# Optimization experiments

Measured on AMD Instinct MI355X. Metric: run time of the kernel, lower is better.

The kernel has to match this reference:

```python
import jax, jax.numpy as jnp
import numpy as np
import math

B, T, V, D, K, H, CH, BN = 8, 1024, 256, 4096, 8192, 512, 8, 256

def setup_inputs() -> dict:
    key = jax.random.key(0)
    ks = jax.random.split(key, 20)
    def n(k, shape, s=0.02):
        return jax.random.normal(k, shape, dtype=jnp.float32) * s
    cb = jnp.where(jax.random.normal(ks[0], (V, D)) >= 0, 1.0, -1.0).astype(jnp.float32)
    return dict(
        idx=jax.random.randint(ks[1], (B, T), 0, V),
        char_codebook=cb,
        log_decay=jnp.full((D,), math.log(0.95 / 0.05), dtype=jnp.float32),
        gate_w=n(ks[2], (D, 1)), gate_b=jnp.zeros((1,), jnp.float32),
        q_w=n(ks[3], (D, BN)), q_b=jnp.zeros((BN,), jnp.float32),
        k_w=n(ks[4], (D, BN)), k_b=jnp.zeros((BN,), jnp.float32),
        phrase_w=n(ks[5], (D, D)), phrase_b=jnp.zeros((D,), jnp.float32),
        mem_keys=n(ks[6], (K, D)), mem_values=n(ks[7], (K, H)),
        log_beta=jnp.asarray(math.log(D ** 0.5), dtype=jnp.float32),
        proj1_w=n(ks[8], (D, H)), proj1_b=jnp.zeros((H,), jnp.float32),
        proj2_w=n(ks[9], (H, H)), proj2_b=jnp.zeros((H,), jnp.float32),
        phr_proj_w=n(ks[10], (D, H)), phr_proj_b=jnp.zeros((H,), jnp.float32),
        res_embed=n(ks[11], (V, H)), pos_embed=n(ks[12], (1024, H)),
        ln_g=jnp.ones((3 * H,), jnp.float32), ln_b=jnp.zeros((3 * H,), jnp.float32),
        nav_w0=n(ks[13], (3 * H, H)), nav_b0=jnp.zeros((H,), jnp.float32),
        nav_w1=n(ks[14], (H, H)), nav_b1=jnp.zeros((H,), jnp.float32),
        nav_w2=n(ks[15], (H, H)), nav_b2=jnp.zeros((H,), jnp.float32),
        head_w=n(ks[16], (H, V)), head_b=jnp.zeros((V,), jnp.float32),
    )

def reference(idx, char_codebook, log_decay, gate_w, gate_b, q_w, q_b, k_w, k_b,
              phrase_w, phrase_b, mem_keys, mem_values, log_beta,
              proj1_w, proj1_b, proj2_w, proj2_b, phr_proj_w, phr_proj_b,
              res_embed, pos_embed, ln_g, ln_b, nav_w0, nav_b0, nav_w1, nav_b1,
              nav_w2, nav_b2, head_w, head_b):
    gelu = lambda x: jax.nn.gelu(x, approximate=False)  # torch nn.GELU default (erf)
    # ---- trigram encoding: bind current char with rolled prev chars ----
    chars = char_codebook[idx]                                   # (B,T,D)
    c1 = jnp.roll(chars, 1, axis=1).at[:, 0, :].set(0.0)
    c2 = jnp.roll(chars, 2, axis=1).at[:, :2, :].set(0.0)
    tri = chars * jnp.roll(c1, 1, axis=-1) * jnp.roll(c2, 2, axis=-1)
    hdc = 0.7 * tri + 0.3 * chars
    # ---- build_context: gate + causal decay matrix + hetero resonance ----
    imp = jax.nn.sigmoid(hdc @ gate_w + gate_b)                  # (B,T,1)
    gated = hdc * imp
    ldr = jnp.mean(jax.nn.log_sigmoid(log_decay))
    i = jnp.arange(T)
    # faithful to source: diffs[t,s] = clamp(s - t, 0) -> tril of exp(ldr*0)=1
    diffs = jnp.clip(i[None, :] - i[:, None], 0, None).astype(jnp.float32)
    dm = jnp.tril(jnp.exp(ldr * diffs))
    dm = dm / (dm.sum(-1, keepdims=True) + 1e-8)                 # (T,T)
    local = jnp.einsum('ts,bsd->btd', dm, gated)
    q = gated @ q_w + q_b                                        # (B,T,BN)
    k = gated @ k_w + k_b
    scores = jnp.einsum('btc,bsc->bts', q, k) * (BN ** -0.5)
    res_mask = i[None, :] <= (i[:, None] - 4)                    # tril diagonal=-4
    scores = jnp.where(res_mask[None], scores, -65000.0)
    resonance = jax.nn.softmax(scores, axis=-1)
    combined = 0.7 * dm[None] + 0.3 * resonance
    hetero = jnp.einsum('bts,bsd->btd', combined, gated)
    contexts = 0.6 * local + 0.4 * hetero + hdc                  # (B,T,D)
    # ---- phrase level: chunk-8 pool, proj, causal decay over chunks ----
    nC = T // CH
    phrase = contexts.reshape(B, nC, CH, D).mean(2) @ phrase_w + phrase_b
    p = jnp.arange(nC)
    pdiff = jnp.clip(p[:, None] - p[None, :], 0, None).astype(jnp.float32)
    pm = jnp.tril(0.9 ** pdiff)
    pm = pm / pm.sum(-1, keepdims=True)
    phrase_ctx = jnp.einsum('ts,bsd->btd', pm, phrase)
    phrase_tok = jnp.repeat(phrase_ctx, CH, axis=1)              # (B,T,D)
    # ---- 3-step iterative Hopfield retrieval over codebook ----
    beta = jnp.exp(log_beta)
    qh = contexts
    for _ in range(3):
        attn = jax.nn.softmax(jnp.einsum('btd,kd->btk', qh, mem_keys) * beta, axis=-1)
        qh = jnp.einsum('btk,kd->btd', attn, mem_keys)
    retrieved = jnp.einsum('btk,kh->bth', attn, mem_values)      # (B,T,H)
    # ---- features + navigator (eval: dropout identity, n_thoughts=1) ----
    f_char = gelu(contexts @ proj1_w + proj1_b) @ proj2_w + proj2_b + retrieved
    f_phr = phrase_tok @ phr_proj_w + phr_proj_b
    f_res = res_embed[idx] + pos_embed[:T][None]
    x = jnp.concatenate([f_char, f_phr, f_res], axis=-1)         # (B,T,3H)
    mu = x.mean(-1, keepdims=True)
    var = ((x - mu) ** 2).mean(-1, keepdims=True)
    xh = (x - mu) / jnp.sqrt(var + 1e-5) * ln_g + ln_b
    h = gelu(xh @ nav_w0 + nav_b0)
    h = gelu(h @ nav_w1 + nav_b1)
    h = gelu(h @ nav_w2 + nav_b2)
    return h @ head_w + head_b                                   # (B,T,V)
```

## Files before the change

kernel.cpp:

```cpp
#include <hip/hip_runtime.h>
#include <cstdint>
#include <cstddef>


using u16 = unsigned short;
typedef __bf16 bf16x8 __attribute__((ext_vector_type(8)));
typedef float  f32x4  __attribute__((ext_vector_type(4)));

#define DEV __device__ __forceinline__

DEV float u2f(u16 u) { return __uint_as_float(((unsigned)u) << 16); }
DEV u16   f2u(float f) {
    unsigned x = __float_as_uint(f);
    return (u16)((x + 0x7fffu + ((x >> 16) & 1u)) >> 16);
}
DEV float gelu_f(float v) { return 0.5f * v * (1.0f + erff(v * 0.70710678118654752440f)); }

enum : int { Tt_ = 1024, Dd_ = 4096, Kk_ = 8192, Hh_ = 512, NC_ = 128, H3_ = 1536 };

template<int OUTK, int BIAS, int GELU, int ADD, int AS, int BS, int BTR>
__global__ __launch_bounds__(256) void gemm_u(
    const void* __restrict__ Av, const void* __restrict__ Av2, long sA, int ldA,
    const void* __restrict__ Bv, const void* __restrict__ Bv2, long sB, int ldB,
    void* __restrict__ Cv, void* __restrict__ Cv2, long sC, int ldC,
// ... 135 lines not shown
        #pragma unroll
        for (int n = 0; n < 4; ++n)
            bh[n] = *(const bf16x8*)&Bs_hi[(wc * 64 + n * 16 + fr) * 32 + fq * 8];
        if constexpr (AS >= 2) {
            #pragma unroll
            for (int m = 0; m < 4; ++m)
                al[m] = *(const bf16x8*)&As_lo[(wr * 64 + m * 16 + fr) * 32 + fq * 8];
        }
        if constexpr (BS >= 2) {
            #pragma unroll
            for (int n = 0; n < 4; ++n)
                bl[n] = *(const bf16x8*)&Bs_lo[(wc * 64 + n * 16 + fr) * 32 + fq * 8];
        }
        #pragma unroll
        for (int m = 0; m < 4; ++m)
            #pragma unroll
            for (int n = 0; n < 4; ++n)
                acc[m][n] = __builtin_amdgcn_mfma_f32_16x16x32_bf16(ah[m], bh[n], acc[m][n], 0, 0, 0);
        if constexpr (AS >= 2) {
            #pragma unroll
            for (int m = 0; m < 4; ++m)
                #pragma unroll
                for (int n = 0; n < 4; ++n)
                    acc[m][n] = __builtin_amdgcn_mfma_f32_16x16x32_bf16(al[m], bh[n], acc[m][n], 0, 0, 0);
        }
        if constexpr (BS >= 2) {
            #pragma unroll
            for (int m = 0; m < 4; ++m)
                #pragma unroll
                for (int n = 0; n < 4; ++n)
                    acc[m][n] = __builtin_amdgcn_mfma_f32_16x16x32_bf16(ah[m], bl[n], acc[m][n], 0, 0, 0);
        }
        __syncthreads();
    }

    float alf = alpha;
    if (alpha_exp) alf *= expf(*alpha_exp);
    const long r0 = arow0 + wr * 64;
    const int  c0 = (int)brow0 + wc * 64;
    const long cbase = (long)blockIdx.z * sC;
    const long dbase = (long)blockIdx.z * sAdd;
    float* Cf = (float*)Cv;
    u16*   Ch = (u16*)Cv;
    u16*   Cl = (u16*)Cv2;
    #pragma unroll
    for (int m = 0; m < 4; ++m) {
        #pragma unroll
        for (int n = 0; n < 4; ++n) {
            const int c = c0 + n * 16 + fr;
            #pragma unroll
            for (int i = 0; i < 4; ++i) {
                const long r = r0 + m * 16 + fq * 4 + i;
                float v = acc[m][n][i] * alf;
                if (BIAS == 1) v += bias[c];
                if (BIAS == 2) v += bias[r];
                if (ADD)  v += addsrc[dbase + r * (long)ldC + c];
                if (GELU) v = gelu_f(v);
                const long o = cbase + r * (long)ldC + c;
                if (OUTK == 0) Cf[o] = v;
                else if (OUTK == 1) Ch[o] = f2u(v);
                else { const u16 h = f2u(v); Ch[o] = h; Cl[o] = f2u(v - u2f(h)); }
            }
        }
    }
}

__global__ __launch_bounds__(256) void gemm_sym(
    const u16* __restrict__ A, u16* __restrict__ G, int N, int Kc)
{
    __shared__ u16 As[128 * 32];
    __shared__ u16 Bs[128 * 32];
    __shared__ u16 tile[128][129];

    int f = blockIdx.x;
    {
        const int nwg = gridDim.x;
        if (nwg >= 16) {
            const int q = nwg >> 3, r = nwg & 7;
            const int xcd = f & 7, pos = f >> 3;
            f = (xcd < r) ? (xcd * (q + 1) + pos)
                          : (r * (q + 1) + (xcd - r) * q + pos);
        }
    }
    int bx = (int)((sqrtf(8.f * (float)f + 1.f) - 1.f) * 0.5f);
    while ((bx + 1) * (bx + 2) / 2 <= f) ++bx;
    while (bx * (bx + 1) / 2 > f) --bx;
    const int by = f - bx * (bx + 1) / 2;

    const int tid = threadIdx.x, lane = tid & 63, wave = tid >> 6;
    const int wr = wave >> 1, wc = wave & 1;
    const int fr = lane & 15, fq = lane >> 4;
    const int srow = tid >> 2, scol = (tid & 3) << 3;
    const u16* Ab = A + ((long)bx * 128 + srow) * Kc + scol;
    const u16* Bg = A + ((long)by * 128 + srow) * Kc + scol;
    u16* asd = &As[srow * 32 + scol];
    u16* bsd = &Bs[srow * 32 + scol];

    f32x4 acc[4][4] = {};
    for (int k0 = 0; k0 < Kc; k0 += 32) {
        __builtin_amdgcn_global_load_lds((const __attribute__((address_space(1))) void*)(Ab + k0),
                                         (__attribute__((address_space(3))) void*)asd, 16, 0, 0);
        __builtin_amdgcn_global_load_lds((const __attribute__((address_space(1))) void*)(Ab + k0 + (long)64 * Kc),
                                         (__attribute__((address_space(3))) void*)(asd + 64 * 32), 16, 0, 0);
        __builtin_amdgcn_global_load_lds((const __attribute__((address_space(1))) void*)(Bg + k0),
                                         (__attribute__((address_space(3))) void*)bsd, 16, 0, 0);
        __builtin_amdgcn_global_load_lds((const __attribute__((address_space(1))) void*)(Bg + k0 + (long)64 * Kc),
                                         (__attribute__((address_space(3))) void*)(bsd + 64 * 32), 16, 0, 0);
        __syncthreads();
        bf16x8 af[4], bv[4];
        #pragma unroll
        for (int m = 0; m < 4; ++m)
            af[m] = *(const bf16x8*)&As[(wr * 64 + m * 16 + fr) * 32 + fq * 8];
        #pragma unroll
        for (int n = 0; n < 4; ++n)
            bv[n] = *(const bf16x8*)&Bs[(wc * 64 + n * 16 + fr) * 32 + fq * 8];
        #pragma unroll
        for (int m = 0; m < 4; ++m)
            #pragma unroll
            for (int n = 0; n < 4; ++n)
                acc[m][n] = __builtin_amdgcn_mfma_f32_16x16x32_bf16(af[m], bv[n], acc[m][n], 0, 0, 0);
        __syncthreads();
    }

    const long rB = (long)bx * 128, cB = (long)by * 128;
    #pragma unroll
    for (int m = 0; m < 4; ++m) {
        #pragma unroll
        for (int n = 0; n < 4; ++n) {
            const int cl = wc * 64 + n * 16 + fr;
            #pragma unroll
            for (int i = 0; i < 4; ++i) {
                const int rl = wr * 64 + m * 16 + fq * 4 + i;
                const u16 h = f2u(acc[m][n][i]);
                G[(rB + rl) * (long)N + cB + cl] = h;
                tile[rl][cl] = h;
            }
        }
    }
    if (bx != by) {
        __syncthreads();
        const int rl2 = (tid & 63) * 2;
        #pragma unroll
        for (int j = 0; j < 32; ++j) {
            const int cl2 = (tid >> 6) + j * 4;
            const unsigned v = (unsigned)tile[rl2][cl2] | ((unsigned)tile[rl2 + 1][cl2] << 16);
            *(unsigned*)&G[(cB + cl2) * (long)N + rB + rl2] = v;
        }
    }
}

__global__ __launch_bounds__(256) void transpose_cast(
    const float* __restrict__ src, u16* __restrict__ dst, int R, int C)
{
    __shared__ float tile[32][33];
    const int c0 = blockIdx.x * 32, r0 = blockIdx.y * 32;
    const int tx = threadIdx.x & 31, ty = threadIdx.x >> 5;
    #pragma unroll
    for (int i = ty; i < 32; i += 8)
        tile[i][tx] = src[(long)(r0 + i) * C + c0 + tx];
    __syncthreads();
    #pragma unroll
    for (int i = ty; i < 32; i += 8)
        dst[(long)(c0 + i) * R + r0 + tx] = f2u(tile[tx][i]);
}

__global__ __launch_bounds__(256) void transpose_split(
    const float* __restrict__ src, u16* __restrict__ dhi, u16* __restrict__ dlo,
    int R, int C)
{
    __shared__ float tile[32][33];
// ... 59 lines not shown
        const float s0 = c0[d];
        float tri = 0.f;
        if (i2 >= 0) {
            const float s1 = c1[(d + Dd_ - 1) & (Dd_ - 1)];
            const float s2 = c2[(d + Dd_ - 2) & (Dd_ - 1)];
            tri = s0 * s1 * s2;
        }
        const float h = 0.7f * tri + 0.3f * s0;
        hv[j] = h;
        part += h * gate_w[d];
    }
    red[threadIdx.x] = part; __syncthreads();
    for (int q = 128; q > 0; q >>= 1) { if (threadIdx.x < q) red[threadIdx.x] += red[threadIdx.x + q]; __syncthreads(); }
    const float imp = 1.f / (1.f + expf(-(red[0] + gate_b[0])));
    if (threadIdx.x == 0) impOut[n] = imp;
    #pragma unroll
    for (int j = 0; j < 16; ++j) {
        const int d = threadIdx.x + j * 256;
        const float v = hv[j] * imp;
        const u16 h = f2u(v);
        gh[(long)n * Dd_ + d] = h;
        gl[(long)n * Dd_ + d] = f2u(v - u2f(h));
    }
}

__global__ __launch_bounds__(256) void seg_sum_pair(
    const u16* __restrict__ gh, const u16* __restrict__ gl, float* __restrict__ segsum)
{
    const int d = blockIdx.x * 256 + threadIdx.x;
    const int seg = blockIdx.y;
    const int b = blockIdx.z;
    const long base = ((long)b * Tt_ + seg * 64) * Dd_ + d;
    float s = 0.f;
    #pragma unroll 8
    for (int r = 0; r < 64; ++r) s += u2f(gh[base + (long)r * Dd_]) + u2f(gl[base + (long)r * Dd_]);
    segsum[((long)b * 16 + seg) * Dd_ + d] = s;
}

__global__ __launch_bounds__(256) void cum_base(
    const u16* __restrict__ gh, const u16* __restrict__ gl,
    const float* __restrict__ segsum, const float* __restrict__ imp,
    float* __restrict__ base, int b0)
{
    const int d = blockIdx.x * 256 + threadIdx.x;
    const int seg = blockIdx.y;
    const int b = b0 + blockIdx.z;
    float acc = 0.f;
    for (int s = 0; s < seg; ++s) acc += segsum[((long)b * 16 + s) * Dd_ + d];
    const long gbase = ((long)b * Tt_ + seg * 64) * Dd_ + d;
    const float* impb = imp + b * Tt_ + seg * 64;
    float* o = base + ((long)blockIdx.z * Tt_ + seg * 64) * Dd_ + d;
    for (int r = 0; r < 64; ++r) {
        const float g = u2f(gh[gbase + (long)r * Dd_]) + u2f(gl[gbase + (long)r * Dd_]);
        acc += g;
        const int t = seg * 64 + r;
        const float local = acc / (float)(t + 1);
        o[(long)r * Dd_] = g / impb[r] + 0.88f * local;
    }
}

__global__ __launch_bounds__(256) void softmax_res_pair(
    const float* __restrict__ scores, u16* __restrict__ rh, u16* __restrict__ rl)
{
    __shared__ float ex[Tt_];
    __shared__ float red[256];
    const int row = blockIdx.x;
    const int t = row & (Tt_ - 1);
    const int tid = threadIdx.x;
    const float* s = scores + (long)row * Tt_;
    u16* oh = rh + (long)row * Tt_;
    u16* ol = rl + (long)row * Tt_;
    if (t < 4) {
        const u16 u = f2u(1.f / 1024.f);
        for (int j = tid; j < Tt_; j += 256) { oh[j] = u; ol[j] = 0; }
        return;
    }
    const int nv = t - 3;
    float mx = -3.0e38f;
    for (int j = tid; j < nv; j += 256) { float v = s[j]; ex[j] = v; mx = fmaxf(mx, v); }
    red[tid] = mx; __syncthreads();
    for (int q = 128; q > 0; q >>= 1) { if (tid < q) red[tid] = fmaxf(red[tid], red[tid + q]); __syncthreads(); }
    const float MX = red[0]; __syncthreads();
    float sum = 0.f;
    for (int j = tid; j < nv; j += 256) { float e = expf(ex[j] - MX); ex[j] = e; sum += e; }
    red[tid] = sum; __syncthreads();
    for (int q = 128; q > 0; q >>= 1) { if (tid < q) red[tid] += red[tid + q]; __syncthreads(); }
    const float inv = 1.f / red[0];
    for (int j = tid; j < nv; j += 256) {
        const float p = ex[j] * inv;
        const u16 h = f2u(p);
        oh[j] = h; ol[j] = f2u(p - u2f(h));
    }
    for (int j = nv + tid; j < Tt_; j += 256) { oh[j] = 0; ol[j] = 0; }
}

__global__ __launch_bounds__(256) void diag_k(
    const float* __restrict__ mk, float* __restrict__ dex)
{
    __shared__ float red[256];
    const int row = blockIdx.x;
    const float* src = mk + (long)row * Dd_;
    float s = 0.f;
    #pragma unroll
    for (int j = 0; j < 16; ++j) { const float x = src[threadIdx.x + j * 256]; s += x * x; }
    red[threadIdx.x] = s; __syncthreads();
    for (int q = 128; q > 0; q >>= 1) { if (threadIdx.x < q) red[threadIdx.x] += red[threadIdx.x + q]; __syncthreads(); }
    if (threadIdx.x == 0) dex[row] = red[0];
}

__global__ __launch_bounds__(256) void select_refine(
    const float* __restrict__ S, const u16* __restrict__ chi,
    const u16* __restrict__ clo, const float* __restrict__ mk,
    const float* __restrict__ log_beta,
    int* __restrict__ cnt, int* __restrict__ idxb, float* __restrict__ wb)
{
    __shared__ float ex[Kk_];
    __shared__ float red[256];
    __shared__ int   ridx[256];
    __shared__ int   cidx[128];
    __shared__ float ce[128];
    __shared__ int   ccnt_s;
    const int tid = threadIdx.x;
    const int row = blockIdx.x;
    const float* s = S + (long)row * Kk_;
    float mx = -3.0e38f; int mi = 0;
    for (int j = tid; j < Kk_; j += 256) {
        const float v = s[j]; ex[j] = v;
        if (v > mx) { mx = v; mi = j; }
    }
    red[tid] = mx; ridx[tid] = mi; __syncthreads();
    for (int q = 128; q > 0; q >>= 1) {
        if (tid < q) {
            if (red[tid + q] > red[tid] ||
                (red[tid + q] == red[tid] && ridx[tid + q] < ridx[tid])) {
                red[tid] = red[tid + q]; ridx[tid] = ridx[tid + q];
            }
        }
        __syncthreads();
    }
    const float MXH = red[0];
    const int   AMX = ridx[0];
    __syncthreads();
    if (tid == 0) cidx[0] = AMX;
    if (tid < 64) {
        int c = 1;
        for (int base = 0; base < Kk_; base += 64) {
            const int col = base + tid;
            const bool keep = (ex[col] >= MXH - 16.0f) && (col != AMX);
            const unsigned long long m = __ballot(keep);
            if (keep) {
                const int pos = c + (int)__popcll(m & ((1ull << tid) - 1ull));
                if (pos < 128) cidx[pos] = col;
            }
            c += (int)__popcll(m);
        }
        if (tid == 0) ccnt_s = (c < 128) ? c : 128;
    }
    __syncthreads();
    const int kc = ccnt_s;
    const long cb = (long)row * Dd_;
    float av[16];
    #pragma unroll
    for (int j = 0; j < 16; ++j) {
        const int d = tid + j * 256;
        av[j] = u2f(chi[cb + d]) + u2f(clo[cb + d]);
    }
    const float beta = expf(*log_beta);
    for (int i = 0; i < kc; ++i) {
        const float* kr = mk + (long)cidx[i] * Dd_;
        float p = 0.f;
        #pragma unroll
        for (int j = 0; j < 16; ++j) p += av[j] * kr[tid + j * 256];
        red[tid] = p; __syncthreads();
        for (int q = 128; q > 0; q >>= 1) { if (tid < q) red[tid] += red[tid + q]; __syncthreads(); }
        if (tid == 0) ce[i] = beta * red[0];
        __syncthreads();
    }
    red[tid] = (tid < kc) ? ce[tid] : -3.0e38f;
    __syncthreads();
    for (int q = 128; q > 0; q >>= 1) { if (tid < q) red[tid] = fmaxf(red[tid], red[tid + q]); __syncthreads(); }
    const float M = red[0]; __syncthreads();
    float sum = 0.f;
    for (int j = tid; j < Kk_; j += 256) sum += expf(ex[j] - M);
    red[tid] = sum; __syncthreads();
    for (int q = 128; q > 0; q >>= 1) { if (tid < q) red[tid] += red[tid + q]; __syncthreads(); }
    float D = red[0]; __syncthreads();
    red[tid] = (tid < kc) ? (expf(ce[tid] - M) - expf(ex[cidx[tid]] - M)) : 0.f;
    __syncthreads();
    for (int q = 128; q > 0; q >>= 1) { if (tid < q) red[tid] += red[tid + q]; __syncthreads(); }
    D += red[0];
    const float invD = 1.f / D;
    if (tid < 64) {
        int c = 0;
        int*   oi = idxb + (long)row * 64;
        float* ow = wb   + (long)row * 64;
        for (int base = 0; base < 128; base += 64) {
            const int i = base + tid;
            const float w = (i < kc) ? expf(ce[i] - M) * invD : 0.f;
            const bool keep = (w > 1e-4f);
            const unsigned long long m = __ballot(keep);
            if (keep) {
                const int pos = c + (int)__popcll(m & ((1ull << tid) - 1ull));
                if (pos < 64) { oi[pos] = cidx[i]; ow[pos] = w; }
            }
            c += (int)__popcll(m);
        }
        if (tid == 0) cnt[row] = (c < 64) ? c : 64;
    }
}

__global__ __launch_bounds__(256) void gram_iter(
    const int* __restrict__ cntI, const int* __restrict__ idxI,
    const float* __restrict__ wI, const u16* __restrict__ G,
    const float* __restrict__ dex, const float* __restrict__ log_beta,
    int* __restrict__ cntO, int* __restrict__ idxO, float* __restrict__ wO)
{
    __shared__ float ex[Kk_];
    __shared__ float red[256];
    const int row = blockIdx.x;
    const int tid = threadIdx.x;
    const float beta = expf(*log_beta);
    const int k = cntI[row];
    float v[32];
    #pragma unroll
    for (int j = 0; j < 32; ++j) v[j] = 0.f;
    for (int i = 0; i < k; ++i) {
        const int   id = idxI[row * 64 + i];
        const float w  = wI[row * 64 + i];
        const u16* g = G + (long)id * Kk_;
        #pragma unroll
        for (int j = 0; j < 32; ++j)
            v[j] += w * u2f(g[tid + j * 256]);
    }
    #pragma unroll
    for (int j = 0; j < 32; ++j) ex[tid + j * 256] = beta * v[j];
    __syncthreads();
    if (tid < k) {
        const int   id = idxI[row * 64 + tid];
        const float w  = wI[row * 64 + tid];
        ex[id] += beta * w * (dex[id] - u2f(G[(long)id * Kk_ + id]));
    }
    __syncthreads();
    float mx = -3.0e38f;
    #pragma unroll
    for (int j = 0; j < 32; ++j) mx = fmaxf(mx, ex[tid + j * 256]);
    red[tid] = mx; __syncthreads();
    for (int q = 128; q > 0; q >>= 1) { if (tid < q) red[tid] = fmaxf(red[tid], red[tid + q]); __syncthreads(); }
    const float MX = red[0]; __syncthreads();
    float sum = 0.f;
    #pragma unroll
    for (int j = 0; j < 32; ++j) {
        const float e = expf(ex[tid + j * 256] - MX);
        ex[tid + j * 256] = e;
        sum += e;
    }
    red[tid] = sum; __syncthreads();
    for (int q = 128; q > 0; q >>= 1) { if (tid < q) red[tid] += red[tid + q]; __syncthreads(); }
    const float inv = 1.f / red[0];
    if (tid < 64) {
        int c = 0;
        int*   oi = idxO + row * 64;
        float* ow = wO   + row * 64;
        for (int base = 0; base < Kk_; base += 64) {
            const float w = ex[base + tid] * inv;
            const bool  keep = (w > 1e-4f);
            const unsigned long long m = __ballot(keep);
            if (keep) {
                const int pos = c + (int)__popcll(m & ((1ull << tid) - 1ull));
                if (pos < 64) { oi[pos] = base + tid; ow[pos] = w; }
            }
            c += (int)__popcll(m);
        }
        if (tid == 0) cntO[row] = (c < 64) ? c : 64;
    }
}

__global__ __launch_bounds__(256) void gather_value(
    const int* __restrict__ cnt, const int* __restrict__ idxb,
    const float* __restrict__ wb, const float* __restrict__ mv,
    float* __restrict__ fchar)
{
    const int row = blockIdx.x;
    const int k = cnt[row];
    float a0 = 0.f, a1 = 0.f;
    for (int i = 0; i < k; ++i) {
        const int   id = idxb[row * 64 + i];
        const float w  = wb[row * 64 + i];
        const float* src = mv + (long)id * Hh_;
        a0 += w * src[threadIdx.x];
        a1 += w * src[threadIdx.x + 256];
    }
    float* o = fchar + (long)row * Hh_;
    o[threadIdx.x]       += a0;
    o[threadIdx.x + 256] += a1;
}

__global__ __launch_bounds__(256) void hdc_gate(
    const int* __restrict__ idx, const float* __restrict__ cb,
    const float* __restrict__ gate_w, const float* __restrict__ gate_b,
    float* __restrict__ gated, int b)
{
    __shared__ float red[256];
    const int t = blockIdx.x;
    const int n = b * Tt_ + t;
    const int i0 = idx[n];
    const int i2 = (t >= 2) ? idx[n - 2] : -1;
    const int i1 = (t >= 1) ? idx[n - 1] : 0;
    const float* c0 = cb + (long)i0 * Dd_;
    const float* c1 = cb + (long)i1 * Dd_;
    const float* c2 = (i2 >= 0) ? cb + (long)i2 * Dd_ : cb;
    float hv[16];
    float part = 0.f;
    #pragma unroll
    for (int j = 0; j < 16; ++j) {
        const int d = threadIdx.x + j * 256;
        const float s0 = c0[d];
        float tri = 0.f;
        if (i2 >= 0) {
            const float s1 = c1[(d + Dd_ - 1) & (Dd_ - 1)];
            const float s2 = c2[(d + Dd_ - 2) & (Dd_ - 1)];
            tri = s0 * s1 * s2;
        }
        const float h = 0.7f * tri + 0.3f * s0;
        hv[j] = h;
        part += h * gate_w[d];
    }
    red[threadIdx.x] = part; __syncthreads();
    for (int q = 128; q > 0; q >>= 1) { if (threadIdx.x < q) red[threadIdx.x] += red[threadIdx.x + q]; __syncthreads(); }
    const float imp = 1.f / (1.f + expf(-(red[0] + gate_b[0])));
    #pragma unroll
    for (int j = 0; j < 16; ++j) {
        const int d = threadIdx.x + j * 256;
        gated[(long)t * Dd_ + d] = hv[j] * imp;
    }
}
// ... 175 lines not shown
    for (int j = tid; j < H3_; j += 256) { float d0 = xs[j] - mu; v += d0 * d0; }
    red[tid] = v; __syncthreads();
    for (int q = 128; q > 0; q >>= 1) { if (tid < q) red[tid] += red[tid + q]; __syncthreads(); }
    const float rstd = rsqrtf(red[0] * (1.f / (float)H3_) + 1e-5f);
    u16* xo = x + (long)n * H3_;
    for (int j = tid; j < H3_; j += 256)
        xo[j] = f2u((xs[j] - mu) * rstd * ln_g[j] + ln_b[j]);
}

__global__ void fill_sentinel(float* o, long n, float val) {
    long i = (long)blockIdx.x * 256 + threadIdx.x;
    if (i < n) o[i] = val;
}

template<int OUTK, int BIAS, int GELU, int ADD, int AS, int BS, int BTR>
static void gemm(hipStream_t st,
                 const void* A, const void* A2, long sA, int ldA,
                 const void* B, const void* B2, long sB, int ldB,
                 void* C, void* C2, long sC, int ldC,
                 const float* bias, const float* add, long sAdd,
                 int M, int Ncols, int Kc, int batch, float alpha, const float* aexp)
{
    dim3 g(M / 128, Ncols / 128, batch), blk(256, 1, 1);
    gemm_u<OUTK, BIAS, GELU, ADD, AS, BS, BTR><<<g, blk, 0, st>>>(
        A, A2, sA, ldA, B, B2, sB, ldB, C, C2, sC, ldC, bias, add, sAdd, Kc, alpha, aexp);
}

struct Args {
    const int* idx; const float* cb;
    const float* gate_w; const float* gate_b;
    const float* q_w; const float* q_b; const float* k_w; const float* k_b;
    const float* phrase_w; const float* phrase_b;
    const float* mem_keys; const float* mem_values; const float* log_beta;
    const float* proj1_w; const float* proj1_b;
    const float* proj2_w; const float* proj2_b;
    const float* phr_proj_w; const float* phr_proj_b;
    const float* res_embed; const float* pos_embed;
    const float* ln_g; const float* ln_b;
    const float* nav_w0; const float* nav_b0;
    const float* nav_w1; const float* nav_b1;
    const float* nav_w2; const float* nav_b2;
    const float* head_w; const float* head_b;
};

static void run_fast(const Args& a, void* d_out, char* ws, hipStream_t stream)
{
    const size_t MB = 1048576;
    u16* p1T    = (u16*)(ws + 0 * MB);
    u16* ppT    = (u16*)(ws + 4 * MB);
    u16* p2T    = (u16*)(ws + 8 * MB);
    u16* n0T    = (u16*)(ws + 8 * MB + 524288);
    u16* n1T    = (u16*)(ws + 10 * MB);
    u16* n2T    = (u16*)(ws + 10 * MB + 524288);
    u16* hT     = (u16*)(ws + 11 * MB);
    float* qkb  = (float*)(ws + 11 * MB + 524288);
    u16* qkwTh  = (u16*)(ws + 12 * MB);
    u16* qkwTl  = (u16*)(ws + 16 * MB);
    float* fphr  = (float*)(ws + 20 * MB);
    float* fchar = (float*)(ws + 22 * MB);
    u16* gb_hi  = (u16*)(ws + 38 * MB);
    u16* gb_lo  = (u16*)(ws + 102 * MB);
    u16* ctx_hi = gb_hi;
    u16* ctx_lo = gb_lo;
    u16* gbT_hi = (u16*)(ws + 166 * MB);
    u16* gbT_lo = (u16*)(ws + 230 * MB);
    u16* phwT   = (u16*)(ws + 166 * MB);
    u16* mk_hi  = (u16*)(ws + 166 * MB);
    u16* x      = (u16*)(ws + 166 * MB);
    u16* h1     = (u16*)(ws + 190 * MB);
    u16* h2     = (u16*)(ws + 198 * MB);
    u16* h3     = (u16*)(ws + 206 * MB);
    float* qkT   = (float*)(ws + 294 * MB);
    u16*   qk_hi = (u16*)(ws + 310 * MB);
    u16*   qk_lo = (u16*)(ws + 318 * MB);
    float* scores= (float*)(ws + 326 * MB);
    float* segs  = (float*)(ws + 358 * MB);
    u16*   rs_hi = (u16*)(ws + 360 * MB);
    u16*   rs_lo = (u16*)(ws + 376 * MB);
    float* base  = (float*)(ws + 294 * MB);
    u16* pool    = (u16*)(ws + 392 * MB);
    u16* phrase  = (u16*)(ws + 400 * MB);
    u16* pctx    = (u16*)(ws + 408 * MB);
    u16* t1      = (u16*)(ws + 416 * MB);
    float* S     = (float*)(ws + 358 * MB);
    u16*   G     = (u16*)(ws + 294 * MB);
    int*   selcA = (int*)(ws + 424 * MB);
    int*   selcB = (int*)(ws + 424 * MB + 262144);
    int*   seliA = (int*)(ws + 425 * MB);
    float* selwA = (float*)(ws + 427 * MB);
    int*   seliB = (int*)(ws + 429 * MB);
    float* selwB = (float*)(ws + 431 * MB);
    float* dexact= (float*)(ws + 433 * MB);
    float* impA  = (float*)(ws + 433 * MB + 32768);

    transpose_cast<<<dim3(16, 128), 256, 0, stream>>>(a.proj1_w, p1T, 4096, 512);
    transpose_cast<<<dim3(16, 16), 256, 0, stream>>>(a.proj2_w, p2T, 512, 512);
    transpose_cast<<<dim3(16, 128), 256, 0, stream>>>(a.phr_proj_w, ppT, 4096, 512);
    transpose_cast<<<dim3(16, 48), 256, 0, stream>>>(a.nav_w0, n0T, 1536, 512);
    transpose_cast<<<dim3(16, 16), 256, 0, stream>>>(a.nav_w1, n1T, 512, 512);
    transpose_cast<<<dim3(16, 16), 256, 0, stream>>>(a.nav_w2, n2T, 512, 512);
    transpose_cast<<<dim3(8, 16), 256, 0, stream>>>(a.head_w, hT, 512, 256);
    transpose_split<<<dim3(8, 128), 256, 0, stream>>>(a.q_w, qkwTh, qkwTl, 4096, 256);
    transpose_split<<<dim3(8, 128), 256, 0, stream>>>(a.k_w, qkwTh + (size_t)256 * 4096,
                                                      qkwTl + (size_t)256 * 4096, 4096, 256);
    hipMemcpyAsync(qkb, a.q_b, 256 * sizeof(float), hipMemcpyDeviceToDevice, stream);
    hipMemcpyAsync(qkb + 256, a.k_b, 256 * sizeof(float), hipMemcpyDeviceToDevice, stream);

    hdc_gate_pair<<<8192, 256, 0, stream>>>(a.idx, a.cb, a.gate_w, a.gate_b,
                                            gb_hi, gb_lo, impA);
    transpose_b2b<<<dim3(128, 32, 8), 256, 0, stream>>>(gb_hi, gbT_hi, 1024, 4096,
                                                        (long)1024 * 4096, (long)4096 * 1024);
    transpose_b2b<<<dim3(128, 32, 8), 256, 0, stream>>>(gb_lo, gbT_lo, 1024, 4096,
                                                        (long)1024 * 4096, (long)4096 * 1024);
    gemm<0, 2, 0, 0, 3, 3, 0>(stream, qkwTh, qkwTl, 0, 4096, gb_hi, gb_lo, 0, 4096,
                              qkT, nullptr, 0, 8192, qkb, nullptr, 0,
                              512, 8192, 4096, 1, 1.0f, nullptr);
    transpose_split<<<dim3(256, 16), 256, 0, stream>>>(qkT, qk_hi, qk_lo, 512, 8192);
    gemm<0, 0, 0, 0, 3, 3, 0>(stream, qk_hi, qk_lo, (long)1024 * 512, 512,
                              qk_hi + 256, qk_lo + 256, (long)1024 * 512, 512,
                              scores, nullptr, (long)1024 * 1024, 1024, nullptr, nullptr, 0,
                              1024, 1024, 256, 8, 0.0625f, nullptr);
    softmax_res_pair<<<8192, 256, 0, stream>>>(scores, rs_hi, rs_lo);
    seg_sum_pair<<<dim3(16, 16, 8), 256, 0, stream>>>(gb_hi, gb_lo, segs);
    for (int h = 0; h < 2; ++h) {
        cum_base<<<dim3(16, 16, 4), 256, 0, stream>>>(gb_hi, gb_lo, segs, impA,
                                                      base, h * 4);
        const long co = (long)h * 4 * 1024 * 4096;
        gemm<2, 0, 0, 1, 3, 3, 0>(stream,
                                  rs_hi + (long)h * 4 * 1024 * 1024,
                                  rs_lo + (long)h * 4 * 1024 * 1024, (long)1024 * 1024, 1024,
                                  gbT_hi + (long)h * 4 * 4096 * 1024,
                                  gbT_lo + (long)h * 4 * 4096 * 1024, (long)4096 * 1024, 1024,
                                  ctx_hi + co, ctx_lo + co, (long)1024 * 4096, 4096,
                                  nullptr, base, (long)1024 * 4096,
                                  1024, 4096, 1024, 4, 0.12f, nullptr);
    }

    pool_b<<<16384, 256, 0, stream>>>(ctx_hi, pool);
    transpose_cast<<<dim3(128, 128), 256, 0, stream>>>(a.phrase_w, phwT, 4096, 4096);
    gemm<1, 1, 0, 0, 0, 0, 0>(stream, pool, nullptr, 0, 4096, phwT, nullptr, 0, 4096,
                              phrase, nullptr, 0, 4096, a.phrase_b, nullptr, 0,
                              1024, 4096, 4096, 1, 1.0f, nullptr);
    phrase_decay<<<128, 256, 0, stream>>>(phrase, pctx);
    gemm<0, 1, 0, 0, 0, 0, 0>(stream, pctx, nullptr, 0, 4096, ppT, nullptr, 0, 4096,
                              fphr, nullptr, 0, 512, a.phr_proj_b, nullptr, 0,
                              1024, 512, 4096, 1, 1.0f, nullptr);

    gemm<1, 1, 1, 0, 0, 0, 0>(stream, ctx_hi, nullptr, 0, 4096, p1T, nullptr, 0, 4096,
                              t1, nullptr, 0, 512, a.proj1_b, nullptr, 0,
                              8192, 512, 4096, 1, 1.0f, nullptr);
    gemm<0, 1, 0, 0, 0, 0, 0>(stream, t1, nullptr, 0, 512, p2T, nullptr, 0, 512,
                              fchar, nullptr, 0, 512, a.proj2_b, nullptr, 0,
                              8192, 512, 512, 1, 1.0f, nullptr);

    cast_hi<<<32768, 256, 0, stream>>>(a.mem_keys, mk_hi, (long)8192 * 4096);
    diag_k<<<8192, 256, 0, stream>>>(a.mem_keys, dexact);

    for (int c = 0; c < 4; ++c) {
        u16* chi = ctx_hi + (long)c * 2048 * 4096;
        u16* clo = ctx_lo + (long)c * 2048 * 4096;
        gemm<0, 0, 0, 0, 0, 0, 0>(stream, chi, nullptr, 0, 4096, mk_hi, nullptr, 0, 4096,
                                  S, nullptr, 0, 8192, nullptr, nullptr, 0,
                                  2048, 8192, 4096, 1, 1.0f, a.log_beta);
        select_refine<<<2048, 256, 0, stream>>>(S, chi, clo, a.mem_keys, a.log_beta,
                                                selcA + c * 2048,
                                                seliA + (long)c * 2048 * 64,
                                                selwA + (long)c * 2048 * 64);
    }

    gemm_sym<<<2080, 256, 0, stream>>>(mk_hi, G, 8192, 4096);
    gram_iter<<<8192, 256, 0, stream>>>(selcA, seliA, selwA, G, dexact, a.log_beta,
                                        selcB, seliB, selwB);
    gram_iter<<<8192, 256, 0, stream>>>(selcB, seliB, selwB, G, dexact, a.log_beta,
                                        selcA, seliA, selwA);
    gather_value<<<8192, 256, 0, stream>>>(selcA, seliA, selwA, a.mem_values, fchar);

    concat_ln<<<8192, 256, 0, stream>>>(fchar, fphr, a.idx, a.res_embed, a.pos_embed,
                                        a.ln_g, a.ln_b, x);
    gemm<1, 1, 1, 0, 0, 0, 0>(stream, x, nullptr, 0, 1536, n0T, nullptr, 0, 1536,
                              h1, nullptr, 0, 512, a.nav_b0, nullptr, 0,
                              8192, 512, 1536, 1, 1.0f, nullptr);
    gemm<1, 1, 1, 0, 0, 0, 0>(stream, h1, nullptr, 0, 512, n1T, nullptr, 0, 512,
                              h2, nullptr, 0, 512, a.nav_b1, nullptr, 0,
                              8192, 512, 512, 1, 1.0f, nullptr);
    gemm<1, 1, 1, 0, 0, 0, 0>(stream, h2, nullptr, 0, 512, n2T, nullptr, 0, 512,
                              h3, nullptr, 0, 512, a.nav_b2, nullptr, 0,
                              8192, 512, 512, 1, 1.0f, nullptr);
    gemm<0, 1, 0, 0, 0, 0, 0>(stream, h3, nullptr, 0, 512, hT, nullptr, 0, 512,
                              d_out, nullptr, 0, 256, a.head_b, nullptr, 0,
                              8192, 256, 512, 1, 1.0f, nullptr);
}

static void run_fallback(const Args& a, void* d_out, char* ws, hipStream_t stream)
{
    const size_t o_p1T   = 0;
    const size_t o_ppT   = 4194304;
    const size_t o_p2T   = 8388608;
    const size_t o_n0T   = 8912896;
    const size_t o_n1T   = 10485760;
    const size_t o_n2T   = 11010048;
    const size_t o_hT    = 11534336;
    const size_t o_fphr  = 11796480;
    const size_t o_fchar = 13893632;
    const size_t o_ctx   = 30670848;
    const size_t o_AR    = 164888576;

    float* ctxf  = (float*)(ws + o_ctx);
    float* fchar = (float*)(ws + o_fchar);
    float* fphr  = (float*)(ws + o_fphr);
    float* gatedb = (float*)(ws + o_AR);
    float* localb = (float*)(ws + o_AR + 16777216);
    float* Rb     = (float*)(ws + o_AR + 33554432);
    float* qf     = (float*)(ws + o_AR + 50331648);
    float* kf     = (float*)(ws + o_AR + 51380224);
    float* segs   = (float*)(ws + o_AR + 52428800);
    float* scores = (float*)(ws + o_AR + 53477376);
    float* reso   = (float*)(ws + o_AR + 57671680);
    u16* pool   = (u16*)(ws + o_AR);
    u16* phrase = (u16*)(ws + o_AR + 8388608);
    u16* pctx   = (u16*)(ws + o_AR + 16777216);
    u16*   t1   = (u16*)(ws + o_AR);
    float* S    = (float*)(ws + o_AR);
    u16*   attn = (u16*)(ws + o_AR + 33554432);
    u16*   x    = (u16*)(ws + o_AR);
    u16*   h1   = (u16*)(ws + o_AR + 25165824);
    u16*   h2   = (u16*)(ws + o_AR + 33554432);
    u16*   h3   = (u16*)(ws + o_AR + 41943040);

    transpose_cast<<<dim3(16, 128), 256, 0, stream>>>(a.proj1_w, (u16*)(ws + o_p1T), 4096, 512);
    transpose_cast<<<dim3(16, 16), 256, 0, stream>>>(a.proj2_w, (u16*)(ws + o_p2T), 512, 512);
    transpose_cast<<<dim3(16, 128), 256, 0, stream>>>(a.phr_proj_w, (u16*)(ws + o_ppT), 4096, 512);
    transpose_cast<<<dim3(16, 48), 256, 0, stream>>>(a.nav_w0, (u16*)(ws + o_n0T), 1536, 512);
    transpose_cast<<<dim3(16, 16), 256, 0, stream>>>(a.nav_w1, (u16*)(ws + o_n1T), 512, 512);
    transpose_cast<<<dim3(16, 16), 256, 0, stream>>>(a.nav_w2, (u16*)(ws + o_n2T), 512, 512);
    transpose_cast<<<dim3(8, 16), 256, 0, stream>>>(a.head_w, (u16*)(ws + o_hT), 512, 256);

    for (int b = 0; b < 8; ++b) {
        hdc_gate<<<1024, 256, 0, stream>>>(a.idx, a.cb, a.gate_w, a.gate_b, gatedb, b);
        gemm<0, 1, 0, 0, 2, 2, 1>(stream, gatedb, nullptr, 0, 4096, a.q_w, nullptr, 0, 256,
                                  qf, nullptr, 0, 256, a.q_b, nullptr, 0,
                                  1024, 256, 4096, 1, 1.0f, nullptr);
        gemm<0, 1, 0, 0, 2, 2, 1>(stream, gatedb, nullptr, 0, 4096, a.k_w, nullptr, 0, 256,
                                  kf, nullptr, 0, 256, a.k_b, nullptr, 0,
                                  1024, 256, 4096, 1, 1.0f, nullptr);
        gemm<0, 0, 0, 0, 2, 2, 0>(stream, qf, nullptr, 0, 256, kf, nullptr, 0, 256,
                                  scores, nullptr, 0, 1024, nullptr, nullptr, 0,
                                  1024, 1024, 256, 1, 0.0625f, nullptr);
        softmax_res<<<1024, 256, 0, stream>>>(scores, reso);
        gemm<0, 0, 0, 0, 2, 2, 1>(stream, reso, nullptr, 0, 1024, gatedb, nullptr, 0, 4096,
                                  Rb, nullptr, 0, 4096, nullptr, nullptr, 0,
                                  1024, 4096, 1024, 1, 1.0f, nullptr);
// ... 116 lines not shown
```

Baseline: 3.164 ms.

## Store Hopfield scores in bf16, merge chunked score GEMM, retile symmetric Gram blocks

The score matrix between contexts and memory keys is now written as bf16 instead of fp32. That halves its size, so the four chunked GEMM plus select_refine passes become one full-batch GEMM and one select_refine launch, with the buffer reusing the Gram region. The symmetric Gram kernel maps block indices through 8x8 super-tiles for better L2 locality, and the softmax paths switch expf to __expf. Because bf16 scores are less precise, the candidate window is widened from 16 to 18 to keep the refinement correct, at some accuracy risk.

```diff
diff --git a/kernel.cpp b/kernel.cpp
--- a/kernel.cpp
+++ b/kernel.cpp
@@ -241,10 +241,27 @@
                           : (r * (q + 1) + (xcd - r) * q + pos);
         }
     }
-    int bx = (int)((sqrtf(8.f * (float)f + 1.f) - 1.f) * 0.5f);
-    while ((bx + 1) * (bx + 2) / 2 <= f) ++bx;
-    while (bx * (bx + 1) / 2 > f) --bx;
-    const int by = f - bx * (bx + 1) / 2;
+    int I = 0, J = 0, local = f;
+    {
+        bool done = false;
+        for (int i = 0; i < 8 && !done; ++i) {
+            for (int j = 0; j <= i; ++j) {
+                const int sz = (i == j) ? 36 : 64;
+                if (local < sz) { I = i; J = j; done = true; break; }
+                local -= sz;
+            }
+        }
+    }
+    int bx, by;
+    if (I == J) {
+        int r = 0;
+        while ((r + 1) * (r + 2) / 2 <= local) ++r;
+        bx = I * 8 + r;
+        by = J * 8 + (local - r * (r + 1) / 2);
+    } else {
+        bx = I * 8 + (local >> 3);
+        by = J * 8 + (local & 7);
+    }
 
     const int tid = threadIdx.x, lane = tid & 63, wave = tid >> 6;
     const int wr = wave >> 1, wc = wave & 1;
@@ -470,7 +487,7 @@
     for (int q = 128; q > 0; q >>= 1) { if (tid < q) red[tid] = fmaxf(red[tid], red[tid + q]); __syncthreads(); }
     const float MX = red[0]; __syncthreads();
     float sum = 0.f;
-    for (int j = tid; j < nv; j += 256) { float e = expf(ex[j] - MX); ex[j] = e; sum += e; }
+    for (int j = tid; j < nv; j += 256) { float e = __expf(ex[j] - MX); ex[j] = e; sum += e; }
     red[tid] = sum; __syncthreads();
     for (int q = 128; q > 0; q >>= 1) { if (tid < q) red[tid] += red[tid + q]; __syncthreads(); }
     const float inv = 1.f / red[0];
@@ -497,7 +514,7 @@
 }
 
 __global__ __launch_bounds__(256) void select_refine(
-    const float* __restrict__ S, const u16* __restrict__ chi,
+    const u16* __restrict__ S, const u16* __restrict__ chi,
     const u16* __restrict__ clo, const float* __restrict__ mk,
     const float* __restrict__ log_beta,
     int* __restrict__ cnt, int* __restrict__ idxb, float* __restrict__ wb)
@@ -510,10 +527,10 @@
     __shared__ int   ccnt_s;
     const int tid = threadIdx.x;
     const int row = blockIdx.x;
-    const float* s = S + (long)row * Kk_;
+    const u16* s = S + (long)row * Kk_;
     float mx = -3.0e38f; int mi = 0;
     for (int j = tid; j < Kk_; j += 256) {
-        const float v = s[j]; ex[j] = v;
+        const float v = u2f(s[j]); ex[j] = v;
         if (v > mx) { mx = v; mi = j; }
     }
     red[tid] = mx; ridx[tid] = mi; __syncthreads();
@@ -534,7 +551,7 @@
         int c = 1;
         for (int base = 0; base < Kk_; base += 64) {
             const int col = base + tid;
-            const bool keep = (ex[col] >= MXH - 16.0f) && (col != AMX);
+            const bool keep = (ex[col] >= MXH - 18.0f) && (col != AMX);
             const unsigned long long m = __ballot(keep);
             if (keep) {
                 const int pos = c + (int)__popcll(m & ((1ull << tid) - 1ull));
@@ -569,11 +586,11 @@
     for (int q = 128; q > 0; q >>= 1) { if (tid < q) red[tid] = fmaxf(red[tid], red[tid + q]); __syncthreads(); }
     const float M = red[0]; __syncthreads();
     float sum = 0.f;
-    for (int j = tid; j < Kk_; j += 256) sum += expf(ex[j] - M);
+    for (int j = tid; j < Kk_; j += 256) sum += __expf(ex[j] - M);
     red[tid] = sum; __syncthreads();
     for (int q = 128; q > 0; q >>= 1) { if (tid < q) red[tid] += red[tid + q]; __syncthreads(); }
     float D = red[0]; __syncthreads();
-    red[tid] = (tid < kc) ? (expf(ce[tid] - M) - expf(ex[cidx[tid]] - M)) : 0.f;
+    red[tid] = (tid < kc) ? (__expf(ce[tid] - M) - __expf(ex[cidx[tid]] - M)) : 0.f;
     __syncthreads();
     for (int q = 128; q > 0; q >>= 1) { if (tid < q) red[tid] += red[tid + q]; __syncthreads(); }
     D += red[0];
@@ -584,7 +601,7 @@
         float* ow = wb   + (long)row * 64;
         for (int base = 0; base < 128; base += 64) {
             const int i = base + tid;
-            const float w = (i < kc) ? expf(ce[i] - M) * invD : 0.f;
+            const float w = (i < kc) ? __expf(ce[i] - M) * invD : 0.f;
             const bool keep = (w > 1e-4f);
             const unsigned long long m = __ballot(keep);
             if (keep) {
@@ -638,7 +655,7 @@
     float sum = 0.f;
     #pragma unroll
     for (int j = 0; j < 32; ++j) {
-        const float e = expf(ex[tid + j * 256] - MX);
+        const float e = __expf(ex[tid + j * 256] - MX);
         ex[tid + j * 256] = e;
         sum += e;
     }
@@ -980,7 +997,7 @@
     u16* phrase  = (u16*)(ws + 400 * MB);
     u16* pctx    = (u16*)(ws + 408 * MB);
     u16* t1      = (u16*)(ws + 416 * MB);
-    float* S     = (float*)(ws + 358 * MB);
+    u16*   S16   = (u16*)(ws + 294 * MB);
     u16*   G     = (u16*)(ws + 294 * MB);
     int*   selcA = (int*)(ws + 424 * MB);
     int*   selcB = (int*)(ws + 424 * MB + 262144);
@@ -1054,17 +1071,11 @@
     cast_hi<<<32768, 256, 0, stream>>>(a.mem_keys, mk_hi, (long)8192 * 4096);
     diag_k<<<8192, 256, 0, stream>>>(a.mem_keys, dexact);
 
-    for (int c = 0; c < 4; ++c) {
-        u16* chi = ctx_hi + (long)c * 2048 * 4096;
-        u16* clo = ctx_lo + (long)c * 2048 * 4096;
-        gemm<0, 0, 0, 0, 0, 0, 0>(stream, chi, nullptr, 0, 4096, mk_hi, nullptr, 0, 4096,
-                                  S, nullptr, 0, 8192, nullptr, nullptr, 0,
-                                  2048, 8192, 4096, 1, 1.0f, a.log_beta);
-        select_refine<<<2048, 256, 0, stream>>>(S, chi, clo, a.mem_keys, a.log_beta,
-                                                selcA + c * 2048,
-                                                seliA + (long)c * 2048 * 64,
-                                                selwA + (long)c * 2048 * 64);
-    }
+    gemm<1, 0, 0, 0, 0, 0, 0>(stream, ctx_hi, nullptr, 0, 4096, mk_hi, nullptr, 0, 4096,
+                              S16, nullptr, 0, 8192, nullptr, nullptr, 0,
+                              8192, 8192, 4096, 1, 1.0f, a.log_beta);
+    select_refine<<<8192, 256, 0, stream>>>(S16, ctx_hi, ctx_lo, a.mem_keys, a.log_beta,
+                                            selcA, seliA, selwA);
 
     gemm_sym<<<2080, 256, 0, stream>>>(mk_hi, G, 8192, 4096);
     gram_iter<<<8192, 256, 0, stream>>>(selcA, seliA, selwA, G, dexact, a.log_beta,
```

Result: faster. 2.963 ms (-6.4%).
